# Performance work log

Measured on AMD Instinct MI355X. Metric: run time of the kernel, lower is better.

## Reference

```python
import jax, jax.numpy as jnp
import numpy as np

B, S, HID = 2, 2048, 2048
NH, HD = 16, 128            # num heads, head dim (HID = NH*HD)
ROT = 64                    # rotary_dim
MASK_VALUE = -10000.0


def _rotate_every_two(x):
    # x: [..., d] with d even; interleaved (-x2, x1)
    x1 = x[..., ::2]
    x2 = x[..., 1::2]
    return jnp.stack((-x2, x1), axis=-1).reshape(x.shape)


def _fixed_sincos(seq_len, dim):
    inv_freq = 1.0 / (10000.0 ** (jnp.arange(0, dim, 2, dtype=jnp.float32) / dim))
    t = jnp.arange(seq_len, dtype=jnp.float32)
    ang = t[:, None] * inv_freq[None, :]          # [S, dim/2]
    return jnp.sin(ang), jnp.cos(ang)


def _apply_rope(x, sin, cos):
    # x: [B, S, H, rot]; sin/cos: [S, rot/2] -> repeat_interleave(2) -> [S, rot]
    sin = jnp.repeat(sin, 2, axis=-1)[None, :, None, :]
    cos = jnp.repeat(cos, 2, axis=-1)[None, :, None, :]
    return x * cos + _rotate_every_two(x) * sin


def setup_inputs() -> dict:
    key = jax.random.key(0)
    ks = jax.random.split(key, 7)
    w_scale = 1.0 / np.sqrt(HID)
    return {
        "hidden_states": jax.random.normal(ks[0], (B, S, HID), dtype=jnp.float32),
        "attention_mask": jnp.zeros((B, 1, 1, S), dtype=jnp.float32),
        "Wq": jax.random.normal(ks[1], (HID, HID), dtype=jnp.float32) * w_scale,
        "bq": jnp.zeros((HID,), dtype=jnp.float32),
        "Wk": jax.random.normal(ks[2], (HID, HID), dtype=jnp.float32) * w_scale,
        "bk": jnp.zeros((HID,), dtype=jnp.float32),
        "Wv": jax.random.normal(ks[3], (HID, HID), dtype=jnp.float32) * w_scale,
        "bv": jnp.zeros((HID,), dtype=jnp.float32),
    }


def reference(hidden_states, attention_mask, Wq, bq, Wk, bk, Wv, bv):
    # QKV projections (torch Linear: x @ W.T + b)
    q = (hidden_states @ Wq.T + bq).reshape(B, S, NH, HD)
    k = (hidden_states @ Wk.T + bk).reshape(B, S, NH, HD)
    v = (hidden_states @ Wv.T + bv).reshape(B, S, NH, HD)

    # Inline rotary on first ROT dims of q/k
    sin, cos = _fixed_sincos(S, ROT)
    q = jnp.concatenate([_apply_rope(q[..., :ROT], sin, cos), q[..., ROT:]], axis=-1)
    k = jnp.concatenate([_apply_rope(k[..., :ROT], sin, cos), k[..., ROT:]], axis=-1)

    # Scores [B, H, S, S]
    scores = jnp.einsum('bqhd,bkhd->bhqk', q, k) / np.sqrt(HD)

    # Causal mask + additive attention mask
    causal = jnp.tril(jnp.ones((S, S), dtype=bool))[None, None]
    scores = jnp.where(causal, scores, jnp.asarray(MASK_VALUE, scores.dtype))
    scores = scores + attention_mask

    probs = jax.nn.softmax(scores, axis=-1)
    ctx = jnp.einsum('bhqk,bkhd->bqhd', probs, v)
    return ctx.reshape(B, S, HID)
```

## Files before the change

### kernel.cpp

```cpp
#include <hip/hip_runtime.h>

typedef unsigned short bhalf;
typedef __attribute__((ext_vector_type(4))) float    f32x4;
typedef __attribute__((ext_vector_type(8))) short    s16x8;
typedef __attribute__((ext_vector_type(4))) float    floatx4;
typedef __attribute__((ext_vector_type(4))) unsigned short u16x4;

#define B_  2
#define S_  2048
#define HID_ 2048
#define NH_ 16
#define HD_ 128
#define M_  (B_*S_)
#define MASKV (-10000.0f)

__device__ __forceinline__ bhalf f32_to_bf16(float f) {
    union { float f; unsigned int u; } v; v.f = f;
    unsigned int r = v.u + 0x7FFFu + ((v.u >> 16) & 1u);
    return (bhalf)(r >> 16);
}
__device__ __forceinline__ bhalf f32_to_bf16_trunc(float f) {
    union { float f; unsigned int u; } v; v.f = f;
    return (bhalf)(v.u >> 16);
}
__device__ __forceinline__ float bf16_to_f32(bhalf h) {
    union { unsigned int u; float f; } v; v.u = ((unsigned int)h) << 16;
    return v.f;
}

__device__ __forceinline__ void gl_lds16(const void* g, void* l) {
    __builtin_amdgcn_global_load_lds(
        (const __attribute__((address_space(1))) void*)g,
        (__attribute__((address_space(3))) void*)l, 16, 0, 0);
}

#define BARRIER() asm volatile("s_barrier" ::: "memory")

__global__ __launch_bounds__(256) void cast_all(const float* __restrict__ hs,
                                                const float* __restrict__ Wq,
                                                const float* __restrict__ Wk,
                                                const float* __restrict__ Wv,
                                                bhalf* __restrict__ dst,
                                                float2* __restrict__ tab) {
    if (blockIdx.x >= 20480) {
        int idx = (blockIdx.x - 20480) * 256 + threadIdx.x;
        int i = idx & 31, s = idx >> 5;
        float inv = expf(-(float)i * 0.2878231366242557f);
        float ang = (float)s * inv;
        tab[idx] = make_float2(sinf(ang), cosf(ang));
        return;
    }
    int idx = blockIdx.x * 256 + threadIdx.x;
    const float* src;
    if (idx < 2097152)      src = hs + (size_t)idx * 4;
    else if (idx < 3145728) src = Wq + (size_t)(idx - 2097152) * 4;
    else if (idx < 4194304) src = Wk + (size_t)(idx - 3145728) * 4;
    else                    src = Wv + (size_t)(idx - 4194304) * 4;
    floatx4 f = *(const floatx4*)src;
    u16x4 o;
    o.x = f32_to_bf16(f.x); o.y = f32_to_bf16(f.y);
    o.z = f32_to_bf16(f.z); o.w = f32_to_bf16(f.w);
    *(u16x4*)(dst + (size_t)idx * 4) = o;
}

__global__ __launch_bounds__(512, 2) void qkv_gemm(const bhalf* __restrict__ A,
                                                   const bhalf* __restrict__ Wb,
                                                   const float* __restrict__ bq,
                                                   const float* __restrict__ bk,
                                                   const float* __restrict__ bv,
                                                   bhalf* __restrict__ Out,
                                                   bhalf* __restrict__ VTo) {
    __shared__ __align__(16) bhalf As[2][16384];
    __shared__ __align__(16) bhalf Bs[2][8192];
    const int tid  = threadIdx.x;
    const int lane = tid & 63, w = tid >> 6;
    const int quad = lane >> 4, l = lane & 15;
    const int wy = w >> 1, wx = w & 1;
    const int m0 = blockIdx.x * 256, n0 = blockIdx.y * 128;
    const int z  = blockIdx.z;
    const bhalf* W    = Wb + (size_t)z * HID_ * HID_;
    const float* bias = (z == 0) ? bq : (z == 1) ? bk : bv;
    bhalf* out        = Out + (size_t)z * M_ * HID_;

    bhalf* AsF = &As[0][0];
    bhalf* BsF = &Bs[0][0];

    const int row_s = tid >> 3;
    const int kg_s  = (tid & 7) ^ (row_s & 7);
    const int w512  = w * 512;

    const bhalf* gA0 = A + (size_t)(m0 +   0 + row_s) * HID_ + kg_s * 8;
    const bhalf* gA1 = A + (size_t)(m0 +  64 + row_s) * HID_ + kg_s * 8;
    const bhalf* gA2 = A + (size_t)(m0 + 128 + row_s) * HID_ + kg_s * 8;
    const bhalf* gA3 = A + (size_t)(m0 + 192 + row_s) * HID_ + kg_s * 8;
    const bhalf* gB0 = W + (size_t)(n0 +   0 + row_s) * HID_ + kg_s * 8;
    const bhalf* gB1 = W + (size_t)(n0 +  64 + row_s) * HID_ + kg_s * 8;

    const int aIdx = (wy * 64 + l) * 64;
    const int bIdx = (wx * 64 + l) * 64;
    const int swz0 = ((0 + quad) ^ (l & 7)) * 8;
    const int swz1 = ((4 + quad) ^ (l & 7)) * 8;

    f32x4 acc[4][4] = {};

#define ADV() do { gA0 += 64; gA1 += 64; gA2 += 64; gA3 += 64;               \
                   gB0 += 64; gB1 += 64; } while (0)

#define KTILE(BUF, ST1, ST2, VM) do {                                        \
    const int CA = (BUF) * 16384, NA = ((BUF) ^ 1) * 16384;                  \
    const int CBB = (BUF) * 8192;                                            \
    s16x8 a_[4][2], b01_[2][2], b23_[2][2];                                  \
              \
    _Pragma("unroll") for (int mt = 0; mt < 4; ++mt) {                       \
        a_[mt][0] = *(const s16x8*)(AsF + CA + aIdx + mt * 1024 + swz0);     \
        a_[mt][1] = *(const s16x8*)(AsF + CA + aIdx + mt * 1024 + swz1); }   \
    _Pragma("unroll") for (int nt = 0; nt < 2; ++nt) {                       \
        b01_[nt][0] = *(const s16x8*)(BsF + CBB + bIdx + nt * 1024 + swz0);  \
        b01_[nt][1] = *(const s16x8*)(BsF + CBB + bIdx + nt * 1024 + swz1); }\
    if (ST1) { gl_lds16(gA2 + 64, AsF + NA + 2 * 4096 + w512);               \
               gl_lds16(gA3 + 64, AsF + NA + 3 * 4096 + w512); }             \
    BARRIER();                                                               \
    __builtin_amdgcn_s_setprio(1);                                           \
    _Pragma("unroll") for (int mt = 0; mt < 2; ++mt)                         \
      _Pragma("unroll") for (int nt = 0; nt < 2; ++nt)                       \
        _Pragma("unroll") for (int ks = 0; ks < 2; ++ks)                     \
          acc[mt][nt] = __builtin_amdgcn_mfma_f32_16x16x32_bf16(             \
              a_[mt][ks], b01_[nt][ks], acc[mt][nt], 0, 0, 0);               \
    __builtin_amdgcn_s_setprio(0);                                           \
    BARRIER();                                                               \
    \
    _Pragma("unroll") for (int nt = 0; nt < 2; ++nt) {                       \
        b23_[nt][0] = *(const s16x8*)(BsF + CBB + bIdx + (nt+2)*1024 + swz0);\
        b23_[nt][1] = *(const s16x8*)(BsF + CBB + bIdx + (nt+2)*1024 + swz1);}\
    if (ST2) { gl_lds16(gA0 + 128, AsF + CA + 0 * 4096 + w512);              \
               gl_lds16(gA1 + 128, AsF + CA + 1 * 4096 + w512); }            \
    BARRIER();                                                               \
    __builtin_amdgcn_s_setprio(1);                                           \
    _Pragma("unroll") for (int mt = 0; mt < 2; ++mt)                         \
      _Pragma("unroll") for (int nt = 0; nt < 2; ++nt)                       \
        _Pragma("unroll") for (int ks = 0; ks < 2; ++ks)                     \
          acc[mt][nt + 2] = __builtin_amdgcn_mfma_f32_16x16x32_bf16(         \
              a_[mt][ks], b23_[nt][ks], acc[mt][nt + 2], 0, 0, 0);           \
    __builtin_amdgcn_s_setprio(0);                                           \
    BARRIER();                                                               \
                  \
    if (ST2) { gl_lds16(gB0 + 128, BsF + CBB + 0 * 4096 + w512);             \
               gl_lds16(gB1 + 128, BsF + CBB + 1 * 4096 + w512); }           \
    BARRIER();                                                               \
    __builtin_amdgcn_s_setprio(1);                                           \
    _Pragma("unroll") for (int mt = 0; mt < 2; ++mt)                         \
      _Pragma("unroll") for (int nt = 0; nt < 2; ++nt)                       \
        _Pragma("unroll") for (int ks = 0; ks < 2; ++ks)                     \
          acc[2 + mt][nt] = __builtin_amdgcn_mfma_f32_16x16x32_bf16(         \
              a_[2 + mt][ks], b01_[nt][ks], acc[2 + mt][nt], 0, 0, 0);       \
    __builtin_amdgcn_s_setprio(0);                                           \
    BARRIER();                                                               \
                           \
    if ((VM) == 4)      asm volatile("s_waitcnt vmcnt(4)" ::: "memory");     \
    else if ((VM) == 0) asm volatile("s_waitcnt vmcnt(0)" ::: "memory");     \
    BARRIER();                                                               \
    __builtin_amdgcn_s_setprio(1);                                           \
    _Pragma("unroll") for (int mt = 0; mt < 2; ++mt)                         \
      _Pragma("unroll") for (int nt = 0; nt < 2; ++nt)                       \
        _Pragma("unroll") for (int ks = 0; ks < 2; ++ks)                     \
          acc[2 + mt][nt + 2] = __builtin_amdgcn_mfma_f32_16x16x32_bf16(     \
              a_[2 + mt][ks], b23_[nt][ks], acc[2 + mt][nt + 2], 0, 0, 0);   \
    __builtin_amdgcn_s_setprio(0);                                           \
    BARRIER();                                                               \
} while (0)

    gl_lds16(gA0, AsF + 0 * 4096 + w512);
    gl_lds16(gA1, AsF + 1 * 4096 + w512);
    gl_lds16(gA2, AsF + 2 * 4096 + w512);
    gl_lds16(gA3, AsF + 3 * 4096 + w512);
    gl_lds16(gB0, BsF + 0 * 4096 + w512);
    gl_lds16(gB1, BsF + 1 * 4096 + w512);
    gl_lds16(gA0 + 64, AsF + 16384 + 0 * 4096 + w512);
    gl_lds16(gA1 + 64, AsF + 16384 + 1 * 4096 + w512);
    gl_lds16(gB0 + 64, BsF + 8192 + 0 * 4096 + w512);
    gl_lds16(gB1 + 64, BsF + 8192 + 1 * 4096 + w512);
    asm volatile("s_waitcnt vmcnt(4)" ::: "memory");
    BARRIER();

    for (int tt = 0; tt < 15; ++tt) {
        KTILE(0, 1, 1, 4); ADV();
        KTILE(1, 1, 1, 4); ADV();
    }
    KTILE(0, 1, 0, 0); ADV();
    KTILE(1, 0, 0, -1);

#undef KTILE
#undef ADV

    if (z == 2) {
#pragma unroll
        for (int mt = 0; mt < 4; ++mt) {
#pragma unroll
            for (int nt = 0; nt < 4; ++nt) {
                int col = n0 + wx * 64 + nt * 16 + l;
                float bv_ = bias[col];
                int row0 = m0 + wy * 64 + mt * 16 + quad * 4;
                int bb = row0 >> 11, s0 = row0 & 2047;
                u16x4 o;
#pragma unroll
                for (int r = 0; r < 4; ++r) o[r] = f32_to_bf16(acc[mt][nt][r] + bv_);
                *(u16x4*)(VTo + ((size_t)(bb * 16) * 128 + col) * S_ + s0) = o;
            }
        }
    } else {
#pragma unroll
        for (int mt = 0; mt < 4; ++mt) {
#pragma unroll
            for (int nt = 0; nt < 4; ++nt) {
                int col = n0 + wx * 64 + nt * 16 + l;
                float bv_ = bias[col];
#pragma unroll
                for (int r = 0; r < 4; ++r) {
                    int row = m0 + wy * 64 + mt * 16 + quad * 4 + r;
                    out[(size_t)row * HID_ + col] = f32_to_bf16(acc[mt][nt][r] + bv_);
                }
            }
        }
    }
}

__global__ __launch_bounds__(256) void rope_apply(bhalf* __restrict__ Qb,
                                                  bhalf* __restrict__ Kb,
                                                  const float2* __restrict__ tab) {
    int flat = blockIdx.x * 256 + threadIdx.x;
    int i = flat & 31;
    int h = (flat >> 5) & 15;
    int s = (flat >> 9) & 2047;
    int b = flat >> 20;
    size_t base = ((size_t)(b * S_ + s)) * HID_ + h * HD_ + 2 * i;
    float2 sc = tab[s * 32 + i];
    float c = sc.y, sn = sc.x;
    {
        unsigned int q = *(const unsigned int*)(Qb + base);
        float x0 = bf16_to_f32((bhalf)(q & 0xffff));
        float x1 = bf16_to_f32((bhalf)(q >> 16));
        unsigned int o = (unsigned int)f32_to_bf16(x0 * c - x1 * sn)
                       | ((unsigned int)f32_to_bf16(x1 * c + x0 * sn) << 16);
        *(unsigned int*)(Qb + base) = o;
    }
    {
        unsigned int k = *(const unsigned int*)(Kb + base);
        float x0 = bf16_to_f32((bhalf)(k & 0xffff));
        float x1 = bf16_to_f32((bhalf)(k >> 16));
        unsigned int o = (unsigned int)f32_to_bf16(x0 * c - x1 * sn)
                       | ((unsigned int)f32_to_bf16(x1 * c + x0 * sn) << 16);
        *(unsigned int*)(Kb + base) = o;
    }
}

__global__ __launch_bounds__(256, 2) void flash_attn(const bhalf* __restrict__ Qb,
                                                     const bhalf* __restrict__ Kb,
                                                     const bhalf* __restrict__ VT,
                                                     const float* __restrict__ amask,
                                                     float* __restrict__ out) {
    __shared__ __align__(16) bhalf Kbuf[2][1024 * 8];
    __shared__ __align__(16) bhalf Vbuf[2][1024 * 8];
    const int tid = threadIdx.x, lane = tid & 63, w = tid >> 6;
    const int quad = lane >> 4, l = lane & 15;
    const int bh = blockIdx.x, pr = blockIdx.y;
    const int b = bh >> 4, h = bh & 15;
    s16x8 ones;
#pragma unroll
    for (int j = 0; j < 8; ++j) ones[j] = (short)0x3F80;
    const int fpl = ((l >> 2) << 1) | (l & 1);

    for (int pass = 0; pass < 2; ++pass) {
        const int qt = pass ? (31 - pr) : pr;
        const int myrow = qt * 64 + w * 16;
        const int nch = qt + 1;

        s16x8 qf[4];
        {
            const bhalf* Qrow = Qb + (size_t)(b * S_ + myrow + l) * HID_ + h * HD_;
#pragma unroll
            for (int ks = 0; ks < 4; ++ks)
                qf[ks] = *(const s16x8*)(Qrow + ks * 32 + quad * 8);
        }

        float m_run[4] = {-1e30f, -1e30f, -1e30f, -1e30f};
        f32x4 l_acc = {};
        f32x4 acc[8] = {};

        __syncthreads();

#pragma unroll
        for (int j = 0; j < 4; ++j) {
            int slot0 = j * 256 + w * 64;
            int slot  = slot0 + lane;
            {
                int row = slot >> 4, x = slot & 15;
                int g   = (x & 8) | ((x ^ row) & 7);
                gl_lds16(Kb + (size_t)(b * S_ + row) * HID_ + h * HD_ + g * 8,
                         &Kbuf[0][slot0 * 8]);
            }
            {
                int row = slot >> 3, x = slot & 7;
                int g   = (x ^ row) & 7;
                gl_lds16(VT + ((size_t)bh * HD_ + row) * S_ + g * 8,
                         &Vbuf[0][slot0 * 8]);
            }
        }

        for (int kc = 0; kc < nch; ++kc) {
            const int cur = kc & 1, nxt = cur ^ 1;
            const int key0 = kc * 64;
            __syncthreads();

            const bool diag = (kc == qt);

            float am[4];
#pragma unroll
            for (int nt = 0; nt < 4; ++nt) am[nt] = amask[b * S_ + key0 + nt * 16 + l];
            if (kc + 1 < nch) {
                const int key1 = key0 + 64;
#pragma unroll
                for (int j = 0; j < 4; ++j) {
                    int slot0 = j * 256 + w * 64;
                    int slot  = slot0 + lane;
                    {
                        int row = slot >> 4, x = slot & 15;
                        int g   = (x & 8) | ((x ^ row) & 7);
                        gl_lds16(Kb + (size_t)(b * S_ + key1 + row) * HID_ + h * HD_ + g * 8,
                                 &Kbuf[nxt][slot0 * 8]);
                    }
                    {
                        int row = slot >> 3, x = slot & 7;
                        int g   = (x ^ row) & 7;
                        gl_lds16(VT + ((size_t)bh * HD_ + row) * S_ + key1 + g * 8,
                                 &Vbuf[nxt][slot0 * 8]);
                    }
                }
            }

            const bhalf* Kc = &Kbuf[cur][0];
            const bhalf* Vc = &Vbuf[cur][0];
            bhalf* Pw = &Kbuf[cur][0] + w * 1024;

            f32x4 s[4] = {};
            __builtin_amdgcn_s_setprio(1);
#pragma unroll
            for (int nt = 0; nt < 4; ++nt) {
                int key = nt * 16 + l;
#pragma unroll
                for (int ks = 0; ks < 4; ++ks) {
                    int dg = ks * 4 + quad;
                    int x  = (dg & 8) | ((dg ^ key) & 7);
                    s16x8 kf = *(const s16x8*)(Kc + (key * 16 + x) * 8);
                    s[nt] = __builtin_amdgcn_mfma_f32_16x16x32_bf16(qf[ks], kf, s[nt], 0, 0, 0);
                }
            }
            __builtin_amdgcn_s_setprio(0);
            __asm__ __volatile__("s_waitcnt lgkmcnt(0)\n\ts_barrier" ::: "memory");

#pragma unroll
            for (int r = 0; r < 4; ++r) {
                const int qrow = myrow + quad * 4 + r;
                float p[4];
#pragma unroll
                for (int nt = 0; nt < 4; ++nt) {
                    float v = s[nt][r] * 0.08838834764831845f;
                    if (diag) { int key = key0 + nt * 16 + l; v = (key > qrow) ? MASKV : v; }
                    p[nt] = v + am[nt];
                }
                float mx = fmaxf(fmaxf(p[0], p[1]), fmaxf(p[2], p[3]));
#pragma unroll
                for (int msk = 1; msk < 16; msk <<= 1) mx = fmaxf(mx, __shfl_xor(mx, msk, 64));
                float m_new = fmaxf(m_run[r], mx);
                float alpha = __expf(m_run[r] - m_new);
                m_run[r] = m_new;
                const int m  = quad * 4 + r;
                const int fm = (quad << 1) | (r & 1);
#pragma unroll
                for (int nt = 0; nt < 4; ++nt) {
                    float e = __expf(p[nt] - m_new);
                    int key = nt * 16 + l;
                    Pw[(m * 8 + ((key >> 3) ^ fm)) * 8 + (key & 7)] = f32_to_bf16_trunc(e);
                }
                l_acc[r] *= alpha;
#pragma unroll
                for (int nt = 0; nt < 8; ++nt) acc[nt][r] *= alpha;
            }
            __builtin_amdgcn_s_setprio(1);
#pragma unroll
            for (int kstep = 0; kstep < 2; ++kstep) {
                int kg = kstep * 4 + quad;
                s16x8 pf = *(const s16x8*)(Pw + (l * 8 + (kg ^ fpl)) * 8);
                l_acc = __builtin_amdgcn_mfma_f32_16x16x32_bf16(pf, ones, l_acc, 0, 0, 0);
#pragma unroll
                for (int nt = 0; nt < 8; ++nt) {
                    int d = nt * 16 + l;
                    int x = (kg ^ d) & 7;
                    s16x8 vf = *(const s16x8*)(Vc + (d * 8 + x) * 8);
                    acc[nt] = __builtin_amdgcn_mfma_f32_16x16x32_bf16(pf, vf, acc[nt], 0, 0, 0);
                }
            }
            __builtin_amdgcn_s_setprio(0);
        }

        float inv[4];
#pragma unroll
        for (int r = 0; r < 4; ++r) inv[r] = 1.f / l_acc[r];
#pragma unroll
        for (int nt = 0; nt < 8; ++nt) {
            int col = h * HD_ + nt * 16 + l;
#pragma unroll
            for (int r = 0; r < 4; ++r)
                out[(size_t)(b * S_ + myrow + quad * 4 + r) * HID_ + col] = acc[nt][r] * inv[r];
        }
    }
}

extern "C" void kernel_launch(void* const* d_in, const int* in_sizes, int n_in,
                              void* d_out, int out_size, void* d_ws, size_t ws_size,
                              hipStream_t stream) {
    const float* hs    = (const float*)d_in[0];
    const float* amask = (const float*)d_in[1];
    const float* Wq    = (const float*)d_in[2];
    const float* bq    = (const float*)d_in[3];
    const float* Wk    = (const float*)d_in[4];
    const float* bk    = (const float*)d_in[5];
    const float* Wv    = (const float*)d_in[6];
    const float* bv    = (const float*)d_in[7];
    float* out = (float*)d_out;

    bhalf* hsb = (bhalf*)d_ws;
    bhalf* wqb = hsb + 8388608;
    bhalf* wkb = wqb + 4194304;
    bhalf* wvb = wkb + 4194304;
    bhalf* Qb  = wvb + 4194304;
    bhalf* Kb  = Qb + 8388608;
    bhalf* VTb = Kb + 8388608;
    float2* tab = (float2*)(VTb + 8388608);

    cast_all<<<20736, 256, 0, stream>>>(hs, Wq, Wk, Wv, hsb, tab);
    qkv_gemm<<<dim3(16, 16, 3), 512, 0, stream>>>(hsb, wqb, bq, bk, bv, Qb, VTb);
    rope_apply<<<8192, 256, 0, stream>>>(Qb, Kb, tab);
    flash_attn<<<dim3(32, 16), 256, 0, stream>>>(Qb, Kb, VTb, amask, out);
}
```

Before: 318.6 us.

## Drop V LDS staging, split causal tile pairs into separate blocks, raise occupancy

The attention kernel no longer stages V^T tiles in shared memory. Each wave now reads its V fragments straight from global memory (expected to hit L2) inside the PV loop, which halves LDS use per block. The paired-pass scheme that balanced causal work is replaced by one query tile per block, with heavy tiles scheduled first, and the grid is doubled. Launch bounds are raised to 4 blocks per SIMD group to hide latency through occupancy. The cost is uncached-by-LDS global loads on the critical MFMA path, and possible register pressure under the tighter bound.

Result: slower. 536.7 us (+68.5%).

```diff
diff --git a/kernel.cpp b/kernel.cpp
--- a/kernel.cpp
+++ b/kernel.cpp
@@ -253,165 +253,142 @@
     }
 }
 
-__global__ __launch_bounds__(256, 2) void flash_attn(const bhalf* __restrict__ Qb,
+__global__ __launch_bounds__(256, 4) void flash_attn(const bhalf* __restrict__ Qb,
                                                      const bhalf* __restrict__ Kb,
                                                      const bhalf* __restrict__ VT,
                                                      const float* __restrict__ amask,
                                                      float* __restrict__ out) {
     __shared__ __align__(16) bhalf Kbuf[2][1024 * 8];
-    __shared__ __align__(16) bhalf Vbuf[2][1024 * 8];
     const int tid = threadIdx.x, lane = tid & 63, w = tid >> 6;
     const int quad = lane >> 4, l = lane & 15;
-    const int bh = blockIdx.x, pr = blockIdx.y;
+    const int bh = blockIdx.x;
+    const int qt = 31 - (int)blockIdx.y;
     const int b = bh >> 4, h = bh & 15;
     s16x8 ones;
 #pragma unroll
     for (int j = 0; j < 8; ++j) ones[j] = (short)0x3F80;
     const int fpl = ((l >> 2) << 1) | (l & 1);
 
-    for (int pass = 0; pass < 2; ++pass) {
-        const int qt = pass ? (31 - pr) : pr;
-        const int myrow = qt * 64 + w * 16;
-        const int nch = qt + 1;
-
-        s16x8 qf[4];
-        {
-            const bhalf* Qrow = Qb + (size_t)(b * S_ + myrow + l) * HID_ + h * HD_;
-#pragma unroll
-            for (int ks = 0; ks < 4; ++ks)
-                qf[ks] = *(const s16x8*)(Qrow + ks * 32 + quad * 8);
-        }
-
-        float m_run[4] = {-1e30f, -1e30f, -1e30f, -1e30f};
-        f32x4 l_acc = {};
-        f32x4 acc[8] = {};
-
+    const int myrow = qt * 64 + w * 16;
+    const int nch = qt + 1;
+    const bhalf* Vbase = VT + (size_t)bh * HD_ * S_;
+
+    s16x8 qf[4];
+    {
+        const bhalf* Qrow = Qb + (size_t)(b * S_ + myrow + l) * HID_ + h * HD_;
+#pragma unroll
+        for (int ks = 0; ks < 4; ++ks)
+            qf[ks] = *(const s16x8*)(Qrow + ks * 32 + quad * 8);
+    }
+
+    float m_run[4] = {-1e30f, -1e30f, -1e30f, -1e30f};
+    f32x4 l_acc = {};
+    f32x4 acc[8] = {};
+
+#pragma unroll
+    for (int j = 0; j < 4; ++j) {
+        int slot0 = j * 256 + w * 64;
+        int slot  = slot0 + lane;
+        int row = slot >> 4, x = slot & 15;
+        int g   = (x & 8) | ((x ^ row) & 7);
+        gl_lds16(Kb + (size_t)(b * S_ + row) * HID_ + h * HD_ + g * 8,
+                 &Kbuf[0][slot0 * 8]);
+    }
+
+    for (int kc = 0; kc < nch; ++kc) {
+        const int cur = kc & 1, nxt = cur ^ 1;
+        const int key0 = kc * 64;
         __syncthreads();
 
-#pragma unroll
-        for (int j = 0; j < 4; ++j) {
-            int slot0 = j * 256 + w * 64;
-            int slot  = slot0 + lane;
-            {
+        const bool diag = (kc == qt);
+
+        float am[4];
+#pragma unroll
+        for (int nt = 0; nt < 4; ++nt) am[nt] = amask[b * S_ + key0 + nt * 16 + l];
+        if (kc + 1 < nch) {
+            const int key1 = key0 + 64;
+#pragma unroll
+            for (int j = 0; j < 4; ++j) {
+                int slot0 = j * 256 + w * 64;
+                int slot  = slot0 + lane;
                 int row = slot >> 4, x = slot & 15;
                 int g   = (x & 8) | ((x ^ row) & 7);
-                gl_lds16(Kb + (size_t)(b * S_ + row) * HID_ + h * HD_ + g * 8,
-                         &Kbuf[0][slot0 * 8]);
-            }
-            {
-                int row = slot >> 3, x = slot & 7;
-                int g   = (x ^ row) & 7;
-                gl_lds16(VT + ((size_t)bh * HD_ + row) * S_ + g * 8,
-                         &Vbuf[0][slot0 * 8]);
-            }
-        }
-
-        for (int kc = 0; kc < nch; ++kc) {
-            const int cur = kc & 1, nxt = cur ^ 1;
-            const int key0 = kc * 64;
-            __syncthreads();
-
-            const bool diag = (kc == qt);
-
-            float am[4];
-#pragma unroll
-            for (int nt = 0; nt < 4; ++nt) am[nt] = amask[b * S_ + key0 + nt * 16 + l];
-            if (kc + 1 < nch) {
-                const int key1 = key0 + 64;
-#pragma unroll
-                for (int j = 0; j < 4; ++j) {
-                    int slot0 = j * 256 + w * 64;
-                    int slot  = slot0 + lane;
-                    {
-                        int row = slot >> 4, x = slot & 15;
-                        int g   = (x & 8) | ((x ^ row) & 7);
-                        gl_lds16(Kb + (size_t)(b * S_ + key1 + row) * HID_ + h * HD_ + g * 8,
-                                 &Kbuf[nxt][slot0 * 8]);
-                    }
-                    {
-                        int row = slot >> 3, x = slot & 7;
-                        int g   = (x ^ row) & 7;
-                        gl_lds16(VT + ((size_t)bh * HD_ + row) * S_ + key1 + g * 8,
-                                 &Vbuf[nxt][slot0 * 8]);
-                    }
-                }
-            }
-
-            const bhalf* Kc = &Kbuf[cur][0];
-            const bhalf* Vc = &Vbuf[cur][0];
-            bhalf* Pw = &Kbuf[cur][0] + w * 1024;
-
-            f32x4 s[4] = {};
-            __builtin_amdgcn_s_setprio(1);
+                gl_lds16(Kb + (size_t)(b * S_ + key1 + row) * HID_ + h * HD_ + g * 8,
+                         &Kbuf[nxt][slot0 * 8]);
+            }
+        }
+
+        const bhalf* Kc = &Kbuf[cur][0];
+        bhalf* Pw = &Kbuf[cur][0] + w * 1024;
+
+        f32x4 s[4] = {};
+        __builtin_amdgcn_s_setprio(1);
+#pragma unroll
+        for (int nt = 0; nt < 4; ++nt) {
+            int key = nt * 16 + l;
+#pragma unroll
+            for (int ks = 0; ks < 4; ++ks) {
+                int dg = ks * 4 + quad;
+                int x  = (dg & 8) | ((dg ^ key) & 7);
+                s16x8 kf = *(const s16x8*)(Kc + (key * 16 + x) * 8);
+                s[nt] = __builtin_amdgcn_mfma_f32_16x16x32_bf16(qf[ks], kf, s[nt], 0, 0, 0);
+            }
+        }
+        __builtin_amdgcn_s_setprio(0);
+        __asm__ __volatile__("s_waitcnt lgkmcnt(0)\n\ts_barrier" ::: "memory");
+
+#pragma unroll
+        for (int r = 0; r < 4; ++r) {
+            const int qrow = myrow + quad * 4 + r;
+            float p[4];
 #pragma unroll
             for (int nt = 0; nt < 4; ++nt) {
+                float v = s[nt][r] * 0.08838834764831845f;
+                if (diag) { int key = key0 + nt * 16 + l; v = (key > qrow) ? MASKV : v; }
+                p[nt] = v + am[nt];
+            }
+            float mx = fmaxf(fmaxf(p[0], p[1]), fmaxf(p[2], p[3]));
+#pragma unroll
+            for (int msk = 1; msk < 16; msk <<= 1) mx = fmaxf(mx, __shfl_xor(mx, msk, 64));
+            float m_new = fmaxf(m_run[r], mx);
+            float alpha = __expf(m_run[r] - m_new);
+            m_run[r] = m_new;
+            const int m  = quad * 4 + r;
+            const int fm = (quad << 1) | (r & 1);
+#pragma unroll
+            for (int nt = 0; nt < 4; ++nt) {
+                float e = __expf(p[nt] - m_new);
                 int key = nt * 16 + l;
-#pragma unroll
-                for (int ks = 0; ks < 4; ++ks) {
-                    int dg = ks * 4 + quad;
-                    int x  = (dg & 8) | ((dg ^ key) & 7);
-                    s16x8 kf = *(const s16x8*)(Kc + (key * 16 + x) * 8);
-                    s[nt] = __builtin_amdgcn_mfma_f32_16x16x32_bf16(qf[ks], kf, s[nt], 0, 0, 0);
-                }
-            }
-            __builtin_amdgcn_s_setprio(0);
-            __asm__ __volatile__("s_waitcnt lgkmcnt(0)\n\ts_barrier" ::: "memory");
-
-#pragma unroll
-            for (int r = 0; r < 4; ++r) {
-                const int qrow = myrow + quad * 4 + r;
-                float p[4];
-#pragma unroll
-                for (int nt = 0; nt < 4; ++nt) {
-                    float v = s[nt][r] * 0.08838834764831845f;
-                    if (diag) { int key = key0 + nt * 16 + l; v = (key > qrow) ? MASKV : v; }
-                    p[nt] = v + am[nt];
-                }
-                float mx = fmaxf(fmaxf(p[0], p[1]), fmaxf(p[2], p[3]));
-#pragma unroll
-                for (int msk = 1; msk < 16; msk <<= 1) mx = fmaxf(mx, __shfl_xor(mx, msk, 64));
-                float m_new = fmaxf(m_run[r], mx);
-                float alpha = __expf(m_run[r] - m_new);
-                m_run[r] = m_new;
-                const int m  = quad * 4 + r;
-                const int fm = (quad << 1) | (r & 1);
-#pragma unroll
-                for (int nt = 0; nt < 4; ++nt) {
-                    float e = __expf(p[nt] - m_new);
-                    int key = nt * 16 + l;
-                    Pw[(m * 8 + ((key >> 3) ^ fm)) * 8 + (key & 7)] = f32_to_bf16_trunc(e);
-                }
-                l_acc[r] *= alpha;
-#pragma unroll
-                for (int nt = 0; nt < 8; ++nt) acc[nt][r] *= alpha;
-            }
-            __builtin_amdgcn_s_setprio(1);
-#pragma unroll
-            for (int kstep = 0; kstep < 2; ++kstep) {
-                int kg = kstep * 4 + quad;
-                s16x8 pf = *(const s16x8*)(Pw + (l * 8 + (kg ^ fpl)) * 8);
-                l_acc = __builtin_amdgcn_mfma_f32_16x16x32_bf16(pf, ones, l_acc, 0, 0, 0);
-#pragma unroll
-                for (int nt = 0; nt < 8; ++nt) {
-                    int d = nt * 16 + l;
-                    int x = (kg ^ d) & 7;
-                    s16x8 vf = *(const s16x8*)(Vc + (d * 8 + x) * 8);
-                    acc[nt] = __builtin_amdgcn_mfma_f32_16x16x32_bf16(pf, vf, acc[nt], 0, 0, 0);
-                }
-            }
-            __builtin_amdgcn_s_setprio(0);
-        }
-
-        float inv[4];
-#pragma unroll
-        for (int r = 0; r < 4; ++r) inv[r] = 1.f / l_acc[r];
-#pragma unroll
-        for (int nt = 0; nt < 8; ++nt) {
-            int col = h * HD_ + nt * 16 + l;
-#pragma unroll
-            for (int r = 0; r < 4; ++r)
-                out[(size_t)(b * S_ + myrow + quad * 4 + r) * HID_ + col] = acc[nt][r] * inv[r];
-        }
+                Pw[(m * 8 + ((key >> 3) ^ fm)) * 8 + (key & 7)] = f32_to_bf16_trunc(e);
+            }
+            l_acc[r] *= alpha;
+#pragma unroll
+            for (int nt = 0; nt < 8; ++nt) acc[nt][r] *= alpha;
+        }
+        __builtin_amdgcn_s_setprio(1);
+#pragma unroll
+        for (int kstep = 0; kstep < 2; ++kstep) {
+            int kg = kstep * 4 + quad;
+            s16x8 pf = *(const s16x8*)(Pw + (l * 8 + (kg ^ fpl)) * 8);
+            l_acc = __builtin_amdgcn_mfma_f32_16x16x32_bf16(pf, ones, l_acc, 0, 0, 0);
+#pragma unroll
+            for (int nt = 0; nt < 8; ++nt) {
+                s16x8 vf = *(const s16x8*)(Vbase + (size_t)(nt * 16 + l) * S_ + key0 + kg * 8);
+                acc[nt] = __builtin_amdgcn_mfma_f32_16x16x32_bf16(pf, vf, acc[nt], 0, 0, 0);
+            }
+        }
+        __builtin_amdgcn_s_setprio(0);
+    }
+
+    float inv[4];
+#pragma unroll
+    for (int r = 0; r < 4; ++r) inv[r] = 1.f / l_acc[r];
+#pragma unroll
+    for (int nt = 0; nt < 8; ++nt) {
+        int col = h * HD_ + nt * 16 + l;
+#pragma unroll
+        for (int r = 0; r < 4; ++r)
+            out[(size_t)(b * S_ + myrow + quad * 4 + r) * HID_ + col] = acc[nt][r] * inv[r];
     }
 }
 
@@ -440,5 +417,5 @@
     cast_all<<<20736, 256, 0, stream>>>(hs, Wq, Wk, Wv, hsb, tab);
     qkv_gemm<<<dim3(16, 16, 3), 512, 0, stream>>>(hsb, wqb, bq, bk, bv, Qb, VTb);
     rope_apply<<<8192, 256, 0, stream>>>(Qb, Kb, tab);
-    flash_attn<<<dim3(32, 16), 256, 0, stream>>>(Qb, Kb, VTb, amask, out);
-}
+    flash_attn<<<dim3(32, 32), 256, 0, stream>>>(Qb, Kb, VTb, amask, out);
+}
```
